# Optimization experiments

Hardware: AMD Instinct MI355X
Metric: run time of the kernel (lower is better)

The kernel has to match this reference:

```python
import jax, jax.numpy as jnp
import numpy as np

NUM_HEADS = 8


def _conv1x1(x, W, b):
    # 1x1 conv == per-pixel linear: x [N,C,H,W], W [O,C], b [O]
    return jnp.einsum('nchw,oc->nohw', x, W) + b[None, :, None, None]


def setup_inputs() -> dict:
    key = jax.random.key(0)
    ks = jax.random.split(key, 10)
    C = 512
    s = 1.0 / np.sqrt(C)  # keep pre-softmax logits in a sane range
    return {
        'x': jax.random.normal(ks[0], (2, C, 64, 64), dtype=jnp.float32),
        'Wq': jax.random.normal(ks[1], (C, C), dtype=jnp.float32) * s,
        'bq': jax.random.normal(ks[2], (C,), dtype=jnp.float32) * 0.01,
        'Wk': jax.random.normal(ks[3], (C, C), dtype=jnp.float32) * s,
        'bk': jax.random.normal(ks[4], (C,), dtype=jnp.float32) * 0.01,
        'Wv': jax.random.normal(ks[5], (C, C), dtype=jnp.float32) * s,
        'bv': jax.random.normal(ks[6], (C,), dtype=jnp.float32) * 0.01,
        'Wo': jax.random.normal(ks[7], (C, C), dtype=jnp.float32) * s,
        'bo': jax.random.normal(ks[8], (C,), dtype=jnp.float32) * 0.01,
        'gamma': jax.random.normal(ks[9], (1,), dtype=jnp.float32),
    }


def reference(x, Wq, bq, Wk, bk, Wv, bv, Wo, bo, gamma):
    N, C, H, W = x.shape
    nh = NUM_HEADS
    hd = C // nh
    S = H * W
    scale = 1.0 / (hd ** 0.5)
    # Projections via 1x1 conv, then split heads over flattened spatial tokens
    Q = _conv1x1(x, Wq, bq).reshape(N, nh, hd, S).transpose(0, 1, 3, 2)  # [N,h,S,d]
    K = _conv1x1(x, Wk, bk).reshape(N, nh, hd, S)                         # [N,h,d,S]
    V = _conv1x1(x, Wv, bv).reshape(N, nh, hd, S).transpose(0, 1, 3, 2)  # [N,h,S,d]
    attn = jax.nn.softmax(jnp.einsum('nhsd,nhdt->nhst', Q, K) * scale, axis=-1)
    out = jnp.einsum('nhst,nhtd->nhsd', attn, V)                          # [N,h,S,d]
    out = out.transpose(0, 1, 3, 2).reshape(N, C, H, W)
    out = _conv1x1(out, Wo, bo)
    return gamma[0] * out + x
```

## Files before the change

### kernel.cpp

```cpp
#include <hip/hip_runtime.h>
#include <hip/hip_bf16.h>

typedef __attribute__((ext_vector_type(4))) float f32x4;
typedef __attribute__((ext_vector_type(8))) short s16x8;
typedef __attribute__((ext_vector_type(4))) unsigned short us16x4;
typedef __attribute__((ext_vector_type(2))) unsigned int u32x2;

#define C_DIM 512
#define S_DIM 4096
#define NB 2
#define NH 8
#define HD 64

#define QSCALE 0.1803368801111244f

__device__ __forceinline__ unsigned short f2bf(float f) {
    union { float f; unsigned u; } v; v.f = f;
    unsigned r = v.u + 0x7FFFu + ((v.u >> 16) & 1u);
    return (unsigned short)(r >> 16);
}

__device__ __forceinline__ float dev_exp2(float x) {
    float r;
    asm("v_exp_f32 %0, %1" : "=v"(r) : "v"(x));
    return r;
}

__device__ __forceinline__ unsigned cvt_pk_bf16(float lo, float hi) {
    unsigned r;
    asm("v_cvt_pk_bf16_f32 %0, %1, %2" : "=v"(r) : "v"(lo), "v"(hi));
    return r;
}

__global__ __launch_bounds__(256) void wconv_kernel(
    const float* __restrict__ Wq, const float* __restrict__ Wk,
    const float* __restrict__ Wv, const float* __restrict__ Wo,
    unsigned short* __restrict__ Wb) {
    int i = blockIdx.x * 256 + threadIdx.x;
    int y = blockIdx.y;
    const float* src = (y == 0) ? Wq : (y == 1) ? Wk : (y == 2) ? Wv : Wo;
    Wb[(size_t)y * 262144 + i] = f2bf(src[i]);
}

__global__ __launch_bounds__(256) void xpose_kernel(
    const float* __restrict__ x, unsigned short* __restrict__ Xt) {
    __shared__ float tile[32][33];
    int n = blockIdx.z;
    int s0 = blockIdx.x * 32;
    int c0 = blockIdx.y * 32;
    int tx = threadIdx.x & 31;
    int ty = threadIdx.x >> 5;
#pragma unroll
    for (int r = 0; r < 4; ++r) {
        int c = c0 + ty + r * 8;
        tile[ty + r * 8][tx] = x[((size_t)n * C_DIM + c) * S_DIM + s0 + tx];
    }
    __syncthreads();
#pragma unroll
    for (int r = 0; r < 4; ++r) {
        int s = s0 + ty + r * 8;
        Xt[((size_t)n * S_DIM + s) * C_DIM + c0 + tx] = f2bf(tile[tx][ty + r * 8]);
    }
}

__global__ __launch_bounds__(256) void qkv_gemm_kernel(
    const unsigned short* __restrict__ Wb, const unsigned short* __restrict__ Xt,
    const float* __restrict__ bq, const float* __restrict__ bk, const float* __restrict__ bv,
    unsigned short* __restrict__ Qt, unsigned short* __restrict__ Kt,
    unsigned short* __restrict__ Vb) {
    __shared__ unsigned short As[128 * 72];
    __shared__ unsigned short Bs[128 * 72];
    int w = blockIdx.z >> 1;
    int n = blockIdx.z & 1;
    const unsigned short* A = Wb + (size_t)w * 262144;
    const unsigned short* B = Xt + (size_t)n * S_DIM * C_DIM;
    int tid = threadIdx.x;
    int wid = tid >> 6, lane = tid & 63;
    int wm = wid >> 1, wn = wid & 1;
    int lr = lane & 15, lq = lane >> 4;
    int bm = blockIdx.y * 128, bt = blockIdx.x * 128;

    f32x4 zero = {0.f, 0.f, 0.f, 0.f};
    f32x4 acc[4][4];
#pragma unroll
    for (int i = 0; i < 4; ++i)
#pragma unroll
        for (int j = 0; j < 4; ++j) acc[i][j] = zero;

    for (int ks = 0; ks < 8; ++ks) {
#pragma unroll
        for (int q = 0; q < 4; ++q) {
            int cc = tid * 4 + q;
            int row = cc >> 3, col8 = (cc & 7) * 8;
            s16x8 av = *(const s16x8*)(A + (size_t)(bm + row) * C_DIM + ks * 64 + col8);
            *(s16x8*)&As[row * 72 + col8] = av;
            s16x8 bvv = *(const s16x8*)(B + (size_t)(bt + row) * C_DIM + ks * 64 + col8);
            *(s16x8*)&Bs[row * 72 + col8] = bvv;
        }
        __syncthreads();
#pragma unroll
        for (int kk = 0; kk < 2; ++kk) {
            s16x8 af[4], bf[4];
#pragma unroll
            for (int i = 0; i < 4; ++i)
                af[i] = *(const s16x8*)&As[(wm * 64 + i * 16 + lr) * 72 + kk * 32 + lq * 8];
#pragma unroll
            for (int j = 0; j < 4; ++j)
                bf[j] = *(const s16x8*)&Bs[(wn * 64 + j * 16 + lr) * 72 + kk * 32 + lq * 8];
#pragma unroll
            for (int i = 0; i < 4; ++i)
#pragma unroll
                for (int j = 0; j < 4; ++j)
                    acc[i][j] = __builtin_amdgcn_mfma_f32_16x16x32_bf16(af[i], bf[j], acc[i][j], 0, 0, 0);
        }
        __syncthreads();
    }

    const float* bias = (w == 0) ? bq : (w == 1) ? bk : bv;
#pragma unroll
    for (int i = 0; i < 4; ++i) {
        int obase = bm + wm * 64 + i * 16 + lq * 4;
#pragma unroll
        for (int j = 0; j < 4; ++j) {
            int t = bt + wn * 64 + j * 16 + lr;
            if (w == 0) {
                us16x4 pk;
#pragma unroll
                for (int r = 0; r < 4; ++r)
                    pk[r] = f2bf((acc[i][j][r] + bias[obase + r]) * QSCALE);
                int h = obase >> 6, d = obase & 63;
                *(us16x4*)&Qt[(((size_t)(n * NH + h) * S_DIM) + t) * HD + d] = pk;
            } else if (w == 1) {
                us16x4 pk;
#pragma unroll
                for (int r = 0; r < 4; ++r) pk[r] = f2bf(acc[i][j][r] + bias[obase + r]);
                int h = obase >> 6, d = obase & 63;
                *(us16x4*)&Kt[(((size_t)(n * NH + h) * S_DIM) + t) * HD + d] = pk;
            } else {
#pragma unroll
                for (int r = 0; r < 4; ++r) {
                    int o = obase + r;
                    Vb[((size_t)(n * C_DIM + o)) * S_DIM + t] = f2bf(acc[i][j][r] + bias[o]);
                }
            }
        }
    }
}

__global__ __launch_bounds__(512, 4) void attn_kernel(
    const unsigned short* __restrict__ Qt, const unsigned short* __restrict__ Kt,
    const unsigned short* __restrict__ Vb, unsigned short* __restrict__ Ot) {
    __shared__ unsigned short Ks[64 * 72];
    __shared__ unsigned short Vs[64 * 72];
    __shared__ unsigned short Ps[8][16 * 72];
    int tid = threadIdx.x, wid = tid >> 6, lane = tid & 63;
    int lr = lane & 15, lq = lane >> 4;

    int bidl = blockIdx.x;
    int swz = (bidl & 7) * 64 + (bidl >> 3);
    int nh = swz >> 5;
    int qb = swz & 31;
    int n = nh >> 3, h = nh & 7;
    int qrow0 = qb * 128 + wid * 16;

    const unsigned short* Qh = Qt + (size_t)nh * S_DIM * HD;
    const unsigned short* Kh = Kt + (size_t)nh * S_DIM * HD;
    const unsigned short* Vh = Vb + ((size_t)(n * C_DIM + h * HD)) * S_DIM;

    s16x8 qf[2];
#pragma unroll
    for (int kk = 0; kk < 2; ++kk)
        qf[kk] = *(const s16x8*)&Qh[((size_t)(qrow0 + lr)) * HD + kk * 32 + lq * 8];

    f32x4 zero = {0.f, 0.f, 0.f, 0.f};
    f32x4 Oacc[4];
#pragma unroll
    for (int md = 0; md < 4; ++md) Oacc[md] = zero;
    float m_run = -1e30f, l_run = 0.f;

    int srow = tid >> 3, scol = (tid & 7) * 8;

    s16x8 kreg = *(const s16x8*)&Kh[((size_t)srow) * HD + scol];
    s16x8 vreg = *(const s16x8*)&Vh[((size_t)srow) * S_DIM + scol];

    for (int kt = 0; kt < 64; ++kt) {
        *(s16x8*)&Ks[srow * 72 + scol] = kreg;
        *(s16x8*)&Vs[srow * 72 + scol] = vreg;
        __syncthreads();
        if (kt < 63) {
            kreg = *(const s16x8*)&Kh[((size_t)((kt + 1) * 64 + srow)) * HD + scol];
            vreg = *(const s16x8*)&Vh[((size_t)srow) * S_DIM + (kt + 1) * 64 + scol];
        }

        f32x4 s_[4];
#pragma unroll
        for (int jm = 0; jm < 4; ++jm) s_[jm] = zero;
        s16x8 kf[4][2];
#pragma unroll
        for (int jm = 0; jm < 4; ++jm)
#pragma unroll
            for (int kk = 0; kk < 2; ++kk)
                kf[jm][kk] = *(const s16x8*)&Ks[(jm * 16 + lr) * 72 + kk * 32 + lq * 8];
#pragma unroll
        for (int jm = 0; jm < 4; ++jm)
#pragma unroll
            for (int kk = 0; kk < 2; ++kk)
                s_[jm] = __builtin_amdgcn_mfma_f32_16x16x32_bf16(kf[jm][kk], qf[kk], s_[jm], 0, 0, 0);

        float mx = -1e30f;
#pragma unroll
        for (int jm = 0; jm < 4; ++jm)
#pragma unroll
            for (int r = 0; r < 4; ++r) mx = fmaxf(mx, s_[jm][r]);
        mx = fmaxf(mx, __shfl_xor(mx, 16));
        mx = fmaxf(mx, __shfl_xor(mx, 32));
        float mnew = fmaxf(m_run, mx);
        float alpha = dev_exp2(m_run - mnew);
        m_run = mnew;
        float rs = 0.f;
#pragma unroll
        for (int jm = 0; jm < 4; ++jm)
#pragma unroll
            for (int r = 0; r < 4; ++r) {
                float p = dev_exp2(s_[jm][r] - mnew);
                s_[jm][r] = p;
                rs += p;
            }
        rs += __shfl_xor(rs, 16);
        rs += __shfl_xor(rs, 32);
        l_run = l_run * alpha + rs;
#pragma unroll
        for (int md = 0; md < 4; ++md) Oacc[md] *= alpha;

#pragma unroll
        for (int jm = 0; jm < 4; ++jm) {
            u32x2 pk;
            pk[0] = cvt_pk_bf16(s_[jm][0], s_[jm][1]);
            pk[1] = cvt_pk_bf16(s_[jm][2], s_[jm][3]);
            *(u32x2*)&Ps[wid][lr * 72 + jm * 16 + lq * 4] = pk;
        }

        s16x8 pf[2];
#pragma unroll
        for (int kk = 0; kk < 2; ++kk)
            pf[kk] = *(const s16x8*)&Ps[wid][lr * 72 + kk * 32 + lq * 8];
#pragma unroll
        for (int md = 0; md < 4; ++md) {
#pragma unroll
            for (int kk = 0; kk < 2; ++kk) {
                s16x8 vf = *(const s16x8*)&Vs[(md * 16 + lr) * 72 + kk * 32 + lq * 8];
                Oacc[md] = __builtin_amdgcn_mfma_f32_16x16x32_bf16(vf, pf[kk], Oacc[md], 0, 0, 0);
            }
        }
        __syncthreads();
    }

    float inv = 1.f / l_run;
    int q = qrow0 + lr;
#pragma unroll
    for (int md = 0; md < 4; ++md) {
        us16x4 pk;
#pragma unroll
        for (int r = 0; r < 4; ++r) pk[r] = f2bf(Oacc[md][r] * inv);
        *(us16x4*)&Ot[((size_t)n * S_DIM + q) * C_DIM + h * HD + md * 16 + lq * 4] = pk;
    }
}

__global__ __launch_bounds__(256) void out_gemm_kernel(
    const unsigned short* __restrict__ Wb, const unsigned short* __restrict__ Ot,
    const float* __restrict__ bo, const float* __restrict__ gamma,
    const float* __restrict__ xin, float* __restrict__ out) {
    __shared__ unsigned short As[128 * 72];
    __shared__ unsigned short Bs[128 * 72];
    int n = blockIdx.z;
    const unsigned short* A = Wb + (size_t)3 * 262144;
    const unsigned short* B = Ot + (size_t)n * S_DIM * C_DIM;
    int tid = threadIdx.x;
    int wid = tid >> 6, lane = tid & 63;
    int wm = wid >> 1, wn = wid & 1;
    int lr = lane & 15, lq = lane >> 4;
    int bm = blockIdx.y * 128, bt = blockIdx.x * 128;

    f32x4 zero = {0.f, 0.f, 0.f, 0.f};
    f32x4 acc[4][4];
#pragma unroll
    for (int i = 0; i < 4; ++i)
#pragma unroll
        for (int j = 0; j < 4; ++j) acc[i][j] = zero;

    for (int ks = 0; ks < 8; ++ks) {
#pragma unroll
        for (int q = 0; q < 4; ++q) {
            int cc = tid * 4 + q;
            int row = cc >> 3, col8 = (cc & 7) * 8;
            s16x8 av = *(const s16x8*)(A + (size_t)(bm + row) * C_DIM + ks * 64 + col8);
            *(s16x8*)&As[row * 72 + col8] = av;
            s16x8 bvv = *(const s16x8*)(B + (size_t)(bt + row) * C_DIM + ks * 64 + col8);
            *(s16x8*)&Bs[row * 72 + col8] = bvv;
        }
        __syncthreads();
#pragma unroll
        for (int kk = 0; kk < 2; ++kk) {
            s16x8 af[4], bf[4];
#pragma unroll
            for (int i = 0; i < 4; ++i)
                af[i] = *(const s16x8*)&As[(wm * 64 + i * 16 + lr) * 72 + kk * 32 + lq * 8];
#pragma unroll
            for (int j = 0; j < 4; ++j)
                bf[j] = *(const s16x8*)&Bs[(wn * 64 + j * 16 + lr) * 72 + kk * 32 + lq * 8];
#pragma unroll
            for (int i = 0; i < 4; ++i)
#pragma unroll
                for (int j = 0; j < 4; ++j)
                    acc[i][j] = __builtin_amdgcn_mfma_f32_16x16x32_bf16(af[i], bf[j], acc[i][j], 0, 0, 0);
        }
        __syncthreads();
    }

    float g = gamma[0];
#pragma unroll
    for (int i = 0; i < 4; ++i) {
        int obase = bm + wm * 64 + i * 16 + lq * 4;
#pragma unroll
        for (int j = 0; j < 4; ++j) {
            int t = bt + wn * 64 + j * 16 + lr;
#pragma unroll
            for (int r = 0; r < 4; ++r) {
                int o = obase + r;
                size_t idx = ((size_t)(n * C_DIM + o)) * S_DIM + t;
                out[idx] = g * (acc[i][j][r] + bo[o]) + xin[idx];
            }
        }
    }
}

extern "C" void kernel_launch(void* const* d_in, const int* in_sizes, int n_in,
                              void* d_out, int out_size, void* d_ws, size_t ws_size,
                              hipStream_t stream) {
    const float* x  = (const float*)d_in[0];
    const float* Wq = (const float*)d_in[1];
    const float* bq = (const float*)d_in[2];
    const float* Wk = (const float*)d_in[3];
    const float* bk = (const float*)d_in[4];
    const float* Wv = (const float*)d_in[5];
    const float* bv = (const float*)d_in[6];
    const float* Wo = (const float*)d_in[7];
    const float* bo = (const float*)d_in[8];
    const float* gamma = (const float*)d_in[9];
    float* out = (float*)d_out;

    char* ws = (char*)d_ws;
    unsigned short* Wb = (unsigned short*)ws;
    unsigned short* Xt = (unsigned short*)(ws + ((size_t)2  << 20));
    unsigned short* Qt = (unsigned short*)(ws + ((size_t)10 << 20));
    unsigned short* Kt = (unsigned short*)(ws + ((size_t)18 << 20));
    unsigned short* Vb = (unsigned short*)(ws + ((size_t)26 << 20));
    unsigned short* Ot = (unsigned short*)(ws + ((size_t)34 << 20));

    wconv_kernel<<<dim3(1024, 4), 256, 0, stream>>>(Wq, Wk, Wv, Wo, Wb);
    xpose_kernel<<<dim3(128, 16, 2), 256, 0, stream>>>(x, Xt);
    qkv_gemm_kernel<<<dim3(32, 4, 6), 256, 0, stream>>>(Wb, Xt, bq, bk, bv, Qt, Kt, Vb);
    attn_kernel<<<512, 512, 0, stream>>>(Qt, Kt, Vb, Ot);
    out_gemm_kernel<<<dim3(32, 4, 2), 256, 0, stream>>>(Wb, Ot, bo, gamma, x, out);
}
```

Measured before the change: 180.3 us.

## Restructure attention to 32x32 MFMA with register-resident P and lazy rescaling

Rewrites the attention inner loop so each of 4 waves owns 32 query rows and uses 32x32x16 bf16 MFMAs instead of 16x16x32. The probability tile is converted to bf16 and rearranged in registers with v_permlane32_swap instead of a round trip through LDS. K/V shared tiles use an XOR swizzle instead of padding, and the online-softmax rescale is skipped unless the running max grows by more than a threshold. This is meant to cut LDS traffic, shuffles and the per-tile rescale work, at the cost of higher register pressure and fewer threads per block.

```diff
diff --git a/kernel.cpp b/kernel.cpp
--- a/kernel.cpp
+++ b/kernel.cpp
@@ -2,9 +2,10 @@
 #include <hip/hip_bf16.h>
 
 typedef __attribute__((ext_vector_type(4))) float f32x4;
+typedef __attribute__((ext_vector_type(16))) float f32x16;
 typedef __attribute__((ext_vector_type(8))) short s16x8;
 typedef __attribute__((ext_vector_type(4))) unsigned short us16x4;
-typedef __attribute__((ext_vector_type(2))) unsigned int u32x2;
+typedef __attribute__((ext_vector_type(4))) unsigned int u32x4;
 
 #define C_DIM 512
 #define S_DIM 4096
@@ -30,6 +31,13 @@
     unsigned r;
     asm("v_cvt_pk_bf16_f32 %0, %1, %2" : "=v"(r) : "v"(lo), "v"(hi));
     return r;
+}
+
+__device__ __forceinline__ void lane_swap(unsigned& a, unsigned& b) {
+    asm("v_permlane32_swap_b32 %0, %1" : "+v"(a), "+v"(b));
+}
+__device__ __forceinline__ void lane_swapf(float& a, float& b) {
+    asm("v_permlane32_swap_b32 %0, %1" : "+v"(a), "+v"(b));
 }
 
 __global__ __launch_bounds__(256) void wconv_kernel(
@@ -147,123 +155,164 @@
     }
 }
 
-__global__ __launch_bounds__(512, 4) void attn_kernel(
+__global__ __launch_bounds__(256) void attn_kernel(
     const unsigned short* __restrict__ Qt, const unsigned short* __restrict__ Kt,
     const unsigned short* __restrict__ Vb, unsigned short* __restrict__ Ot) {
-    __shared__ unsigned short Ks[64 * 72];
-    __shared__ unsigned short Vs[64 * 72];
-    __shared__ unsigned short Ps[8][16 * 72];
+    __shared__ unsigned short Ks[64 * 64];
+    __shared__ unsigned short Vs[64 * 64];
     int tid = threadIdx.x, wid = tid >> 6, lane = tid & 63;
-    int lr = lane & 15, lq = lane >> 4;
+    int l31 = lane & 31, hi = lane >> 5;
 
     int bidl = blockIdx.x;
     int swz = (bidl & 7) * 64 + (bidl >> 3);
     int nh = swz >> 5;
     int qb = swz & 31;
     int n = nh >> 3, h = nh & 7;
-    int qrow0 = qb * 128 + wid * 16;
+    int qrow0 = qb * 128 + wid * 32;
 
     const unsigned short* Qh = Qt + (size_t)nh * S_DIM * HD;
     const unsigned short* Kh = Kt + (size_t)nh * S_DIM * HD;
     const unsigned short* Vh = Vb + ((size_t)(n * C_DIM + h * HD)) * S_DIM;
 
-    s16x8 qf[2];
-#pragma unroll
-    for (int kk = 0; kk < 2; ++kk)
-        qf[kk] = *(const s16x8*)&Qh[((size_t)(qrow0 + lr)) * HD + kk * 32 + lq * 8];
-
-    f32x4 zero = {0.f, 0.f, 0.f, 0.f};
-    f32x4 Oacc[4];
-#pragma unroll
-    for (int md = 0; md < 4; ++md) Oacc[md] = zero;
+    s16x8 qf[4];
+#pragma unroll
+    for (int s = 0; s < 4; ++s)
+        qf[s] = *(const s16x8*)&Qh[((size_t)(qrow0 + l31)) * HD + s * 16 + hi * 8];
+
+    f32x16 Oacc[2];
+#pragma unroll
+    for (int jm = 0; jm < 2; ++jm)
+#pragma unroll
+        for (int r = 0; r < 16; ++r) Oacc[jm][r] = 0.f;
     float m_run = -1e30f, l_run = 0.f;
 
-    int srow = tid >> 3, scol = (tid & 7) * 8;
-
-    s16x8 kreg = *(const s16x8*)&Kh[((size_t)srow) * HD + scol];
-    s16x8 vreg = *(const s16x8*)&Vh[((size_t)srow) * S_DIM + scol];
+    int srow0 = tid >> 3, sslot = tid & 7;
+
+    s16x8 kreg[2], vreg[2];
+#pragma unroll
+    for (int q = 0; q < 2; ++q) {
+        int row = srow0 + q * 32;
+        kreg[q] = *(const s16x8*)&Kh[((size_t)row) * HD + sslot * 8];
+        vreg[q] = *(const s16x8*)&Vh[((size_t)row) * S_DIM + sslot * 8];
+    }
 
     for (int kt = 0; kt < 64; ++kt) {
-        *(s16x8*)&Ks[srow * 72 + scol] = kreg;
-        *(s16x8*)&Vs[srow * 72 + scol] = vreg;
+#pragma unroll
+        for (int q = 0; q < 2; ++q) {
+            int row = srow0 + q * 32;
+            int ws = (sslot ^ (row & 7)) * 8;
+            *(s16x8*)&Ks[row * 64 + ws] = kreg[q];
+            *(s16x8*)&Vs[row * 64 + ws] = vreg[q];
+        }
         __syncthreads();
         if (kt < 63) {
-            kreg = *(const s16x8*)&Kh[((size_t)((kt + 1) * 64 + srow)) * HD + scol];
-            vreg = *(const s16x8*)&Vh[((size_t)srow) * S_DIM + (kt + 1) * 64 + scol];
-        }
-
-        f32x4 s_[4];
-#pragma unroll
-        for (int jm = 0; jm < 4; ++jm) s_[jm] = zero;
-        s16x8 kf[4][2];
-#pragma unroll
-        for (int jm = 0; jm < 4; ++jm)
-#pragma unroll
-            for (int kk = 0; kk < 2; ++kk)
-                kf[jm][kk] = *(const s16x8*)&Ks[(jm * 16 + lr) * 72 + kk * 32 + lq * 8];
-#pragma unroll
-        for (int jm = 0; jm < 4; ++jm)
-#pragma unroll
-            for (int kk = 0; kk < 2; ++kk)
-                s_[jm] = __builtin_amdgcn_mfma_f32_16x16x32_bf16(kf[jm][kk], qf[kk], s_[jm], 0, 0, 0);
-
-        float mx = -1e30f;
-#pragma unroll
-        for (int jm = 0; jm < 4; ++jm)
-#pragma unroll
-            for (int r = 0; r < 4; ++r) mx = fmaxf(mx, s_[jm][r]);
-        mx = fmaxf(mx, __shfl_xor(mx, 16));
-        mx = fmaxf(mx, __shfl_xor(mx, 32));
-        float mnew = fmaxf(m_run, mx);
-        float alpha = dev_exp2(m_run - mnew);
-        m_run = mnew;
+#pragma unroll
+            for (int q = 0; q < 2; ++q) {
+                int row = srow0 + q * 32;
+                kreg[q] = *(const s16x8*)&Kh[((size_t)((kt + 1) * 64 + row)) * HD + sslot * 8];
+                vreg[q] = *(const s16x8*)&Vh[((size_t)row) * S_DIM + (kt + 1) * 64 + sslot * 8];
+            }
+        }
+
+        f32x16 s_[2];
+#pragma unroll
+        for (int jm = 0; jm < 2; ++jm) {
+#pragma unroll
+            for (int r = 0; r < 16; ++r) s_[jm][r] = 0.f;
+            int arow = jm * 32 + l31;
+            int sw = (arow & 7);
+#pragma unroll
+            for (int st = 0; st < 4; ++st) {
+                s16x8 kf = *(const s16x8*)&Ks[arow * 64 + ((2 * st + hi) ^ sw) * 8];
+                s_[jm] = __builtin_amdgcn_mfma_f32_32x32x16_bf16(kf, qf[st], s_[jm], 0, 0, 0);
+            }
+        }
+
+        float pm = s_[0][0];
+#pragma unroll
+        for (int jm = 0; jm < 2; ++jm)
+#pragma unroll
+            for (int r = 0; r < 16; ++r) pm = fmaxf(pm, s_[jm][r]);
+        {
+            float a = pm, b = pm;
+            lane_swapf(a, b);
+            pm = fmaxf(a, b);
+        }
+        if (__any(pm > m_run + 8.0f)) {
+            float mnew = fmaxf(m_run, pm);
+            float alpha = dev_exp2(m_run - mnew);
+            m_run = mnew;
+            l_run *= alpha;
+#pragma unroll
+            for (int jm = 0; jm < 2; ++jm)
+#pragma unroll
+                for (int r = 0; r < 16; ++r) Oacc[jm][r] *= alpha;
+        }
         float rs = 0.f;
 #pragma unroll
-        for (int jm = 0; jm < 4; ++jm)
-#pragma unroll
-            for (int r = 0; r < 4; ++r) {
-                float p = dev_exp2(s_[jm][r] - mnew);
+        for (int jm = 0; jm < 2; ++jm)
+#pragma unroll
+            for (int r = 0; r < 16; ++r) {
+                float p = dev_exp2(s_[jm][r] - m_run);
                 s_[jm][r] = p;
                 rs += p;
             }
-        rs += __shfl_xor(rs, 16);
-        rs += __shfl_xor(rs, 32);
-        l_run = l_run * alpha + rs;
-#pragma unroll
-        for (int md = 0; md < 4; ++md) Oacc[md] *= alpha;
-
-#pragma unroll
-        for (int jm = 0; jm < 4; ++jm) {
-            u32x2 pk;
-            pk[0] = cvt_pk_bf16(s_[jm][0], s_[jm][1]);
-            pk[1] = cvt_pk_bf16(s_[jm][2], s_[jm][3]);
-            *(u32x2*)&Ps[wid][lr * 72 + jm * 16 + lq * 4] = pk;
-        }
-
-        s16x8 pf[2];
-#pragma unroll
-        for (int kk = 0; kk < 2; ++kk)
-            pf[kk] = *(const s16x8*)&Ps[wid][lr * 72 + kk * 32 + lq * 8];
-#pragma unroll
-        for (int md = 0; md < 4; ++md) {
-#pragma unroll
-            for (int kk = 0; kk < 2; ++kk) {
-                s16x8 vf = *(const s16x8*)&Vs[(md * 16 + lr) * 72 + kk * 32 + lq * 8];
-                Oacc[md] = __builtin_amdgcn_mfma_f32_16x16x32_bf16(vf, pf[kk], Oacc[md], 0, 0, 0);
-            }
+        {
+            float a = rs, b = rs;
+            lane_swapf(a, b);
+            rs = a + b;
+        }
+        l_run += rs;
+
+        s16x8 pf[2][2];
+#pragma unroll
+        for (int jm = 0; jm < 2; ++jm) {
+            unsigned pk0 = cvt_pk_bf16(s_[jm][0],  s_[jm][1]);
+            unsigned pk1 = cvt_pk_bf16(s_[jm][2],  s_[jm][3]);
+            unsigned pk2 = cvt_pk_bf16(s_[jm][4],  s_[jm][5]);
+            unsigned pk3 = cvt_pk_bf16(s_[jm][6],  s_[jm][7]);
+            unsigned pk4 = cvt_pk_bf16(s_[jm][8],  s_[jm][9]);
+            unsigned pk5 = cvt_pk_bf16(s_[jm][10], s_[jm][11]);
+            unsigned pk6 = cvt_pk_bf16(s_[jm][12], s_[jm][13]);
+            unsigned pk7 = cvt_pk_bf16(s_[jm][14], s_[jm][15]);
+            lane_swap(pk2, pk0);
+            lane_swap(pk3, pk1);
+            lane_swap(pk6, pk4);
+            lane_swap(pk7, pk5);
+            u32x4 w0 = {pk0, pk1, pk2, pk3};
+            u32x4 w1 = {pk4, pk5, pk6, pk7};
+            pf[jm][0] = __builtin_bit_cast(s16x8, w0);
+            pf[jm][1] = __builtin_bit_cast(s16x8, w1);
+        }
+
+#pragma unroll
+        for (int jm2 = 0; jm2 < 2; ++jm2) {
+            int vrow = jm2 * 32 + l31;
+            int sw = (vrow & 7);
+#pragma unroll
+            for (int jm = 0; jm < 2; ++jm)
+#pragma unroll
+                for (int st = 0; st < 2; ++st) {
+                    s16x8 vf = *(const s16x8*)&Vs[vrow * 64 + ((jm * 4 + st * 2 + hi) ^ sw) * 8];
+                    Oacc[jm2] = __builtin_amdgcn_mfma_f32_32x32x16_bf16(vf, pf[jm][st], Oacc[jm2], 0, 0, 0);
+                }
         }
         __syncthreads();
     }
 
     float inv = 1.f / l_run;
-    int q = qrow0 + lr;
-#pragma unroll
-    for (int md = 0; md < 4; ++md) {
-        us16x4 pk;
-#pragma unroll
-        for (int r = 0; r < 4; ++r) pk[r] = f2bf(Oacc[md][r] * inv);
-        *(us16x4*)&Ot[((size_t)n * S_DIM + q) * C_DIM + h * HD + md * 16 + lq * 4] = pk;
-    }
+    int token = qrow0 + l31;
+    unsigned short* orow = Ot + ((size_t)n * S_DIM + token) * C_DIM + h * HD;
+#pragma unroll
+    for (int jm2 = 0; jm2 < 2; ++jm2)
+#pragma unroll
+        for (int rq = 0; rq < 4; ++rq) {
+            int d = jm2 * 32 + 8 * rq + 4 * hi;
+            us16x4 pk;
+#pragma unroll
+            for (int r = 0; r < 4; ++r) pk[r] = f2bf(Oacc[jm2][rq * 4 + r] * inv);
+            *(us16x4*)&orow[d] = pk;
+        }
 }
 
 __global__ __launch_bounds__(256) void out_gemm_kernel(
@@ -360,6 +409,6 @@
     wconv_kernel<<<dim3(1024, 4), 256, 0, stream>>>(Wq, Wk, Wv, Wo, Wb);
     xpose_kernel<<<dim3(128, 16, 2), 256, 0, stream>>>(x, Xt);
     qkv_gemm_kernel<<<dim3(32, 4, 6), 256, 0, stream>>>(Wb, Xt, bq, bk, bv, Qt, Kt, Vb);
-    attn_kernel<<<512, 512, 0, stream>>>(Qt, Kt, Vb, Ot);
+    attn_kernel<<<512, 256, 0, stream>>>(Qt, Kt, Vb, Ot);
     out_gemm_kernel<<<dim3(32, 4, 2), 256, 0, stream>>>(Wb, Ot, bo, gamma, x, out);
 }
```

New measurement: 166.7 us. 7.6% less time.
